# Performance work log

Measured on AMD Instinct MI355X. Metric: run time of the kernel, lower is better.

The kernel has to match this reference:

```python
import jax, jax.numpy as jnp
import numpy as np

L, D, H, R = 8, 1024, 16, 16
HD = D // H  # head dim


def setup_inputs() -> dict:
    key = jax.random.key(0)
    ks = jax.random.split(key, 7)
    s = 0.02  # init scale for stability
    return {
        "x": jax.random.normal(ks[0], (2, 1024, D), jnp.float32),
        "Wqkv": jax.random.normal(ks[1], (L, D, 3 * D), jnp.float32) * s,
        "Aqkv": jax.random.normal(ks[2], (L, D, R), jnp.float32) * s,
        "Bqkv": jax.random.normal(ks[3], (L, R, 3 * D), jnp.float32) * s,
        "Wproj": jax.random.normal(ks[4], (L, D, D), jnp.float32) * s,
        "Aproj": jax.random.normal(ks[5], (L, D, R), jnp.float32) * s,
        "Bproj": jax.random.normal(ks[6], (L, R, D), jnp.float32) * s,
    }


def _forward(x, Wqkv, Aqkv, Bqkv, Wproj, Aproj, Bproj):
    B, S, _ = x.shape
    # causal mask [S, S]
    mask = jnp.tril(jnp.ones((S, S), bool))

    def layer(h, p):
        Wq, Aq, Bq, Wp, Ap, Bp = p
        # LoRA merge exactly as the module: p + A @ B, then dense matmul
        Wq_m = Wq + Aq @ Bq            # [D, 3D]
        Wp_m = Wp + Ap @ Bp            # [D, D]
        qkv = h @ Wq_m                 # [B, S, 3D]
        q, k, v = jnp.split(qkv, 3, axis=-1)
        q = q.reshape(B, S, H, HD).transpose(0, 2, 1, 3)  # [B,H,S,hd]
        k = k.reshape(B, S, H, HD).transpose(0, 2, 1, 3)
        v = v.reshape(B, S, H, HD).transpose(0, 2, 1, 3)
        scores = jnp.einsum("bhqd,bhkd->bhqk", q, k) / np.sqrt(HD)
        scores = jnp.where(mask, scores, jnp.finfo(scores.dtype).min)
        attn = jax.nn.softmax(scores, axis=-1)
        o = jnp.einsum("bhqk,bhkd->bhqd", attn, v)        # [B,H,S,hd]
        o = o.transpose(0, 2, 1, 3).reshape(B, S, D)
        return h + o @ Wp_m, None

    out, _ = jax.lax.scan(layer, x, (Wqkv, Aqkv, Bqkv, Wproj, Aproj, Bproj))
    return out


def reference(x, Wqkv, Aqkv, Bqkv, Wproj, Aproj, Bproj):
    return _forward(x, Wqkv, Aqkv, Bqkv, Wproj, Aproj, Bproj)
```

## Files before the change

### kernel.cpp

```cpp
#include <hip/hip_runtime.h>
#include <hip/hip_bf16.h>


typedef unsigned short ushort_t;
typedef __attribute__((ext_vector_type(8))) short bf16x8;
typedef __attribute__((ext_vector_type(4))) float f32x4;

__device__ __forceinline__ unsigned short f2bf(float f) {
    union { float f; unsigned int u; } x; x.f = f;
    unsigned int r = x.u + 0x7fffu + ((x.u >> 16) & 1u);
    return (unsigned short)(r >> 16);
}

__device__ __forceinline__ f32x4 mfma16(bf16x8 a, bf16x8 b, f32x4 c) {
    return __builtin_amdgcn_mfma_f32_16x16x32_bf16(a, b, c, 0, 0, 0);
}

typedef const __attribute__((address_space(1))) unsigned int* gas_ptr;
typedef __attribute__((address_space(3))) unsigned int* las_ptr;
__device__ __forceinline__ void lds_stage16(const void* g, void* l) {
    __builtin_amdgcn_global_load_lds((gas_ptr)(unsigned long long)g,
                                     (las_ptr)(unsigned int)(unsigned long long)l,
                                     16, 0, 0);
}

#define RORMAX(x, C)                                                           \
    x = fmaxf(x, __int_as_float(__builtin_amdgcn_mov_dpp(                      \
                     __float_as_int(x), C, 0xf, 0xf, false)));
#define RORADD(x, C)                                                           \
    x += __int_as_float(__builtin_amdgcn_mov_dpp(                              \
        __float_as_int(x), C, 0xf, 0xf, false));

__global__ __launch_bounds__(256) void convert_x(
    const float4* __restrict__ in, float4* __restrict__ outF,
    ushort4* __restrict__ outB, int n4) {
    int i = blockIdx.x * 256 + threadIdx.x;
    if (i < n4) {
        float4 v = in[i];
        outF[i] = v;
        ushort4 o;
        o.x = f2bf(v.x); o.y = f2bf(v.y); o.z = f2bf(v.z); o.w = f2bf(v.w);
        outB[i] = o;
    }
}

__global__ __launch_bounds__(256) void merge_T2(
    const float* __restrict__ Wq, const float* __restrict__ Aq,
    const float* __restrict__ Bq, unsigned short* __restrict__ WTq,
    const float* __restrict__ Wp, const float* __restrict__ Ap,
    const float* __restrict__ Bp, unsigned short* __restrict__ WTp) {
    __shared__ float Asl[32][17];
    __shared__ __align__(16) float tW[32 * 128];
    int bid = blockIdx.x;
    const float *W, *A, *Bm;
    unsigned short* WT;
    int N, bx, by, bz;
    if (bid < 6144) {
        N = 3072; bx = bid % 24; int u = bid / 24; by = u & 31; bz = u >> 5;
        W = Wq; A = Aq; Bm = Bq; WT = WTq;
    } else {
        bid -= 6144;
        N = 1024; bx = bid & 7; int u = bid >> 3; by = u & 31; bz = u >> 5;
        W = Wp; A = Ap; Bm = Bp; WT = WTp;
    }
    W  += (size_t)bz * 1024 * N;
    A  += (size_t)bz * 1024 * 16;
    Bm += (size_t)bz * 16 * N;
    WT += (size_t)bz * N * 1024;
    const int j0 = bx * 128, i0 = by * 32;
    const int tid = threadIdx.x;
    const int w = tid >> 6, lane = tid & 63;

    #pragma unroll
    for (int s = 0; s < 4; s++) {
        int w4s = w * 4 + s;
        int tr = w4s * 2 + (lane >> 5);
        lds_stage16(W + (size_t)(i0 + tr) * N + j0 + (lane & 31) * 4,
                    (char*)tW + w4s * 1024);
    }
    if (tid < 128) {
        int r = tid >> 2, c4 = (tid & 3) * 4;
        float4 a = *(const float4*)&A[(size_t)(i0 + r) * 16 + c4];
        Asl[r][c4 + 0] = a.x; Asl[r][c4 + 1] = a.y;
        Asl[r][c4 + 2] = a.z; Asl[r][c4 + 3] = a.w;
    }
    const int jj = tid >> 1, half = tid & 1;
    float bcol[16];
    #pragma unroll
    for (int r = 0; r < 16; r++)
        bcol[r] = Bm[(size_t)r * N + j0 + jj];
    __builtin_amdgcn_sched_barrier(0);
    __syncthreads();

    bf16x8 o0, o1;
    #pragma unroll
    for (int c = 0; c < 16; c++) {
        int rloc = half * 16 + c;
        float v = tW[rloc * 128 + jj];
        #pragma unroll
        for (int r = 0; r < 16; r++)
            v += Asl[rloc][r] * bcol[r];
        unsigned short b = f2bf(v);
        if (c < 8) o0[c] = (short)b; else o1[c - 8] = (short)b;
    }
    unsigned short* dst = &WT[(size_t)(j0 + jj) * 1024 + i0 + half * 16];
    *(bf16x8*)dst = o0;
    *(bf16x8*)(dst + 8) = o1;
}

__global__ __launch_bounds__(256) void gemm_qkv(
    const unsigned short* __restrict__ A,
    const unsigned short* __restrict__ BT,
    unsigned short* __restrict__ outB,
    unsigned short* __restrict__ VT,
    int M, int N, int K) {
    __shared__ __align__(16) unsigned short As[2][2][64 * 32];
    __shared__ __align__(16) unsigned short Bs[2][2][128 * 32];
    const int tid = threadIdx.x;
    const int m0 = blockIdx.y * 64, n0 = blockIdx.x * 128;
    const int w = tid >> 6, lane = tid & 63;
    const int wm = (w >> 1) * 32, wn = (w & 1) * 64;
    const int lr = lane & 15, quad = lane >> 4;
    const int srowA = w * 16 + (lane >> 2);
    const int skof = (lane & 3) * 8;

    f32x4 acc[2][4] = {};

    auto stage = [&](int k0, int buf) {
        #pragma unroll
        for (int h = 0; h < 2; h++) {
            lds_stage16(A + (size_t)(m0 + srowA) * K + k0 + h * 32 + skof,
                        (char*)As[buf][h] + w * 1024);
            #pragma unroll
            for (int s = 0; s < 2; s++) {
                int srowB = w * 32 + s * 16 + (lane >> 2);
                lds_stage16(BT + (size_t)(n0 + srowB) * K + k0 + h * 32 + skof,
                            (char*)Bs[buf][h] + (w * 2 + s) * 1024);
            }
        }
    };

    const int nk = K >> 6;
    stage(0, 0);
    for (int t = 0; t < nk; t++) {
        __syncthreads();
        if (t + 1 < nk) stage((t + 1) << 6, (t + 1) & 1);
        const int cur = t & 1;
        #pragma unroll
        for (int h = 0; h < 2; h++) {
            bf16x8 af[2], bfr[4];
            #pragma unroll
            for (int i = 0; i < 2; i++)
                af[i] = *(const bf16x8*)&As[cur][h][(wm + i * 16 + lr) * 32 + quad * 8];
            #pragma unroll
            for (int j = 0; j < 4; j++)
                bfr[j] = *(const bf16x8*)&Bs[cur][h][(wn + j * 16 + lr) * 32 + quad * 8];
            #pragma unroll
            for (int i = 0; i < 2; i++)
                #pragma unroll
                for (int j = 0; j < 4; j++)
                    acc[i][j] = mfma16(af[i], bfr[j], acc[i][j]);
        }
    }
    if (n0 < 2048) {
        #pragma unroll
        for (int i = 0; i < 2; i++)
            #pragma unroll
            for (int j = 0; j < 4; j++)
                #pragma unroll
                for (int r = 0; r < 4; r++) {
                    int row = m0 + wm + i * 16 + quad * 4 + r;
                    int col = n0 + wn + j * 16 + lr;
                    float v = acc[i][j][r];
                    if (col < 1024) v *= 0.125f * 1.44269504f;
                    outB[(size_t)row * N + col] = f2bf(v);
                }
    } else {
        const int b = m0 >> 10;
        #pragma unroll
        for (int i = 0; i < 2; i++) {
            int row0 = m0 + wm + i * 16 + quad * 4;
            int s = row0 & 1023;
            #pragma unroll
            for (int j = 0; j < 4; j++) {
                int hd = n0 - 2048 + wn + j * 16 + lr;
                ushort4 o;
                o.x = f2bf(acc[i][j][0]); o.y = f2bf(acc[i][j][1]);
                o.z = f2bf(acc[i][j][2]); o.w = f2bf(acc[i][j][3]);
                *(ushort4*)&VT[((size_t)b * 1024 + hd) * 1024 + s] = o;
            }
        }
    }
}

__global__ __launch_bounds__(256) void gemm_bf16_64(
    const unsigned short* __restrict__ A,
    const unsigned short* __restrict__ BT,
    const float* __restrict__ res,
    float* __restrict__ outF,
    unsigned short* __restrict__ outB,
    int M, int N, int K) {
    __shared__ __align__(16) unsigned short As[2][2][64 * 32];
    __shared__ __align__(16) unsigned short Bs[2][2][64 * 32];
    const int tid = threadIdx.x;
    const int m0 = blockIdx.y * 64, n0 = blockIdx.x * 64;
    const int w = tid >> 6, lane = tid & 63;
    const int wm = (w >> 1) * 32, wn = (w & 1) * 32;
    const int lr = lane & 15, quad = lane >> 4;
    const int srow = w * 16 + (lane >> 2);
    const int skof = (lane & 3) * 8;

    f32x4 acc[2][2] = {};

    auto stage = [&](int k0, int buf) {
        #pragma unroll
        for (int h = 0; h < 2; h++) {
            lds_stage16(A  + (size_t)(m0 + srow) * K + k0 + h * 32 + skof,
                        (char*)As[buf][h] + w * 1024);
            lds_stage16(BT + (size_t)(n0 + srow) * K + k0 + h * 32 + skof,
                        (char*)Bs[buf][h] + w * 1024);
        }
    };

    const int nk = K >> 6;
    stage(0, 0);
    for (int t = 0; t < nk; t++) {
        __syncthreads();
        if (t + 1 < nk) stage((t + 1) << 6, (t + 1) & 1);
        const int cur = t & 1;
        #pragma unroll
        for (int h = 0; h < 2; h++) {
            bf16x8 af[2], bfr[2];
            #pragma unroll
            for (int i = 0; i < 2; i++) {
                af[i]  = *(const bf16x8*)&As[cur][h][(wm + i * 16 + lr) * 32 + quad * 8];
                bfr[i] = *(const bf16x8*)&Bs[cur][h][(wn + i * 16 + lr) * 32 + quad * 8];
            }
            #pragma unroll
            for (int i = 0; i < 2; i++)
                #pragma unroll
                for (int j = 0; j < 2; j++)
                    acc[i][j] = mfma16(af[i], bfr[j], acc[i][j]);
        }
    }
    #pragma unroll
    for (int i = 0; i < 2; i++)
        #pragma unroll
        for (int j = 0; j < 2; j++)
            #pragma unroll
            for (int r = 0; r < 4; r++) {
                int row = m0 + wm + i * 16 + quad * 4 + r;
                int col = n0 + wn + j * 16 + lr;
                float v = acc[i][j][r] + res[(size_t)row * N + col];
                if (outF) outF[(size_t)row * N + col] = v;
                if (outB) outB[(size_t)row * N + col] = f2bf(v);
            }
}

__global__ __launch_bounds__(256) void attn_kernel(
    const unsigned short* __restrict__ qkv,
    const unsigned short* __restrict__ VT,
    unsigned short* __restrict__ O) {
    __shared__ __align__(16) unsigned short Ks[2][2][64 * 32];
    __shared__ __align__(16) unsigned short Vs[2][2][64 * 32];
    __shared__ __align__(16) unsigned short pl[4][16 * 72];
    const int tid = threadIdx.x;
    const int w = tid >> 6, lane = tid & 63;
    const int lr = lane & 15, quad = lane >> 4;
    const int bh = blockIdx.y, b = bh >> 4, h = bh & 15;
    const int qblk = (bh < 16) ? blockIdx.x : (15 - blockIdx.x);
    const int qb = qblk * 64 + w * 16;
    const int srow = w * 16 + (lane >> 2);
    const int skof = (lane & 3) * 8;

    const size_t rowQ = (size_t)(b * 1024 + qb + lr) * 3072 + h * 64;
    bf16x8 aq0 = *(const bf16x8*)&qkv[rowQ + quad * 8];
    bf16x8 aq1 = *(const bf16x8*)&qkv[rowQ + 32 + quad * 8];

    float m_i[4], l_i[4];
    f32x4 oacc[4] = {};
    #pragma unroll
    for (int r = 0; r < 4; r++) { m_i[r] = -1e30f; l_i[r] = 0.f; }

    auto stage = [&](int kt64, int buf) {
        const int kt = kt64 << 6;
        const size_t gK = (size_t)(b * 1024 + kt + srow) * 3072 + 1024 + h * 64;
        lds_stage16(qkv + gK + skof,      (char*)Ks[buf][0] + w * 1024);
        lds_stage16(qkv + gK + 32 + skof, (char*)Ks[buf][1] + w * 1024);
        const size_t gV = ((size_t)bh * 64 + srow) * 1024 + kt;
        lds_stage16(VT + gV + skof,       (char*)Vs[buf][0] + w * 1024);
        lds_stage16(VT + gV + 32 + skof,  (char*)Vs[buf][1] + w * 1024);
    };

    const int nkt = qblk + 1;
    stage(0, 0);
    for (int kt64 = 0; kt64 < nkt; kt64++) {
        __syncthreads();
        if (kt64 + 1 < nkt) stage(kt64 + 1, (kt64 + 1) & 1);
        const int cur = kt64 & 1;
        const int kt = kt64 << 6;

        f32x4 s[4] = {};
        #pragma unroll
        for (int nh = 0; nh < 4; nh++) {
            bf16x8 kb0 = *(const bf16x8*)&Ks[cur][0][(nh * 16 + lr) * 32 + quad * 8];
            bf16x8 kb1 = *(const bf16x8*)&Ks[cur][1][(nh * 16 + lr) * 32 + quad * 8];
            s[nh] = mfma16(aq0, kb0, s[nh]);
            s[nh] = mfma16(aq1, kb1, s[nh]);
        }
        float mx[4];
        if (kt + 64 > qb) {
            #pragma unroll
            for (int r = 0; r < 4; r++) {
                int qrow = qb + quad * 4 + r;
                #pragma unroll
                for (int nh = 0; nh < 4; nh++) {
                    int kcol = kt + nh * 16 + lr;
                    s[nh][r] = (kcol <= qrow) ? s[nh][r] : -1e30f;
                }
            }
        }
        #pragma unroll
        for (int r = 0; r < 4; r++) {
            mx[r] = fmaxf(fmaxf(s[0][r], s[1][r]), fmaxf(s[2][r], s[3][r]));
            RORMAX(mx[r], 0x121) RORMAX(mx[r], 0x122)
            RORMAX(mx[r], 0x124) RORMAX(mx[r], 0x128)
        }
        float al[4];
        #pragma unroll
        for (int r = 0; r < 4; r++) {
            float mnew = fmaxf(m_i[r], mx[r]);
            al[r] = exp2f(m_i[r] - mnew);
            m_i[r] = mnew;
            float lsum = 0.f;
            #pragma unroll
            for (int nh = 0; nh < 4; nh++) {
                float p = exp2f(s[nh][r] - mnew);
                s[nh][r] = p;
                lsum += p;
            }
            l_i[r] = l_i[r] * al[r] + lsum;
        }
        #pragma unroll
        for (int dt = 0; dt < 4; dt++)
            #pragma unroll
            for (int r = 0; r < 4; r++) oacc[dt][r] *= al[r];
        #pragma unroll
        for (int nh = 0; nh < 4; nh++)
            #pragma unroll
            for (int r = 0; r < 4; r++)
                pl[w][(quad * 4 + r) * 72 + nh * 16 + lr] = f2bf(s[nh][r]);
        bf16x8 ap0 = *(const bf16x8*)&pl[w][lr * 72 + quad * 8];
        bf16x8 ap1 = *(const bf16x8*)&pl[w][lr * 72 + 32 + quad * 8];
        #pragma unroll
        for (int dt = 0; dt < 4; dt++) {
            bf16x8 vb0 = *(const bf16x8*)&Vs[cur][0][(dt * 16 + lr) * 32 + quad * 8];
            bf16x8 vb1 = *(const bf16x8*)&Vs[cur][1][(dt * 16 + lr) * 32 + quad * 8];
            oacc[dt] = mfma16(ap0, vb0, oacc[dt]);
            oacc[dt] = mfma16(ap1, vb1, oacc[dt]);
        }
    }
    #pragma unroll
    for (int r = 0; r < 4; r++) {
        RORADD(l_i[r], 0x121) RORADD(l_i[r], 0x122)
        RORADD(l_i[r], 0x124) RORADD(l_i[r], 0x128)
    }
    #pragma unroll
    for (int dt = 0; dt < 4; dt++)
        #pragma unroll
        for (int r = 0; r < 4; r++) {
            int row = b * 1024 + qb + quad * 4 + r;
            int col = h * 64 + dt * 16 + lr;
            O[(size_t)row * 1024 + col] = f2bf(oacc[dt][r] / l_i[r]);
        }
}

extern "C" void kernel_launch(void* const* d_in, const int* in_sizes, int n_in,
                              void* d_out, int out_size, void* d_ws, size_t ws_size,
                              hipStream_t stream) {
    const float* x     = (const float*)d_in[0];
    const float* Wqkv  = (const float*)d_in[1];
    const float* Aqkv  = (const float*)d_in[2];
    const float* Bqkv  = (const float*)d_in[3];
    const float* Wproj = (const float*)d_in[4];
    const float* Aproj = (const float*)d_in[5];
    const float* Bproj = (const float*)d_in[6];
    float* out = (float*)d_out;

    char* ws = (char*)d_ws;
    float* h_f32 = (float*)ws;                    ws += (size_t)2048 * 1024 * 4;
    unsigned short* h_bf   = (unsigned short*)ws; ws += (size_t)2048 * 1024 * 2;
    unsigned short* qkv_bf = (unsigned short*)ws; ws += (size_t)2048 * 3072 * 2;
    unsigned short* VT     = (unsigned short*)ws; ws += (size_t)32 * 64 * 1024 * 2;
    unsigned short* O_bf   = (unsigned short*)ws; ws += (size_t)2048 * 1024 * 2;
    unsigned short* WqT8   = (unsigned short*)ws; ws += (size_t)8 * 3072 * 1024 * 2;
    unsigned short* WpT8   = (unsigned short*)ws; ws += (size_t)8 * 1024 * 1024 * 2;

    convert_x<<<2048, 256, 0, stream>>>((const float4*)x, (float4*)h_f32,
                                        (ushort4*)h_bf, 2048 * 1024 / 4);
    merge_T2<<<8192, 256, 0, stream>>>(Wqkv, Aqkv, Bqkv, WqT8,
                                       Wproj, Aproj, Bproj, WpT8);

    for (int l = 0; l < 8; l++) {
        const unsigned short* WqT = WqT8 + (size_t)l * 3072 * 1024;
        const unsigned short* WpT = WpT8 + (size_t)l * 1024 * 1024;
        gemm_qkv<<<dim3(24, 32), 256, 0, stream>>>(h_bf, WqT, qkv_bf, VT,
                                                   2048, 3072, 1024);
        attn_kernel<<<dim3(16, 32), 256, 0, stream>>>(qkv_bf, VT, O_bf);
        float* outF = (l == 7) ? out : h_f32;
        gemm_bf16_64<<<dim3(16, 32), 256, 0, stream>>>(O_bf, WpT, h_f32, outF,
                                                       h_bf, 2048, 1024, 1024);
    }
}
```

Measured before the change: 682.5 us.

## Transpose QK^T MFMA in attention so softmax runs per-lane with lazy rescale

Swaps the MFMA operands for the score product so each lane holds one query row, letting the row max and sum mostly reduce within registers plus two cross-lane shuffles. Adds a threshold-based lazy rescale that skips the output rescale unless the running max grows by more than 8. Packs P to bf16 with the hardware v_cvt_pk_bf16_f32 instruction and writes it as vectors, and replaces the final division with a reciprocal multiply. Skipping the rescale lets exponentials run against a stale max, which relies on fp32 headroom; the attention kernel is only part of the total time.

Measured after the change: 664.2 us. 2.7% less time.

```diff
diff --git a/kernel.cpp b/kernel.cpp
--- a/kernel.cpp
+++ b/kernel.cpp
@@ -5,11 +5,24 @@
 typedef unsigned short ushort_t;
 typedef __attribute__((ext_vector_type(8))) short bf16x8;
 typedef __attribute__((ext_vector_type(4))) float f32x4;
+typedef __attribute__((ext_vector_type(2))) unsigned int uint32x2;
 
 __device__ __forceinline__ unsigned short f2bf(float f) {
     union { float f; unsigned int u; } x; x.f = f;
     unsigned int r = x.u + 0x7fffu + ((x.u >> 16) & 1u);
     return (unsigned short)(r >> 16);
+}
+
+__device__ __forceinline__ unsigned short f2bf_fast(float f) {
+    unsigned int r;
+    asm("v_cvt_pk_bf16_f32 %0, %1, %2" : "=v"(r) : "v"(f), "v"(0.f));
+    return (unsigned short)r;
+}
+
+__device__ __forceinline__ unsigned int cvtpk(float lo, float hi) {
+    unsigned int r;
+    asm("v_cvt_pk_bf16_f32 %0, %1, %2" : "=v"(r) : "v"(lo), "v"(hi));
+    return r;
 }
 
 __device__ __forceinline__ f32x4 mfma16(bf16x8 a, bf16x8 b, f32x4 c) {
@@ -23,13 +36,6 @@
                                      (las_ptr)(unsigned int)(unsigned long long)l,
                                      16, 0, 0);
 }
-
-#define RORMAX(x, C)                                                           \
-    x = fmaxf(x, __int_as_float(__builtin_amdgcn_mov_dpp(                      \
-                     __float_as_int(x), C, 0xf, 0xf, false)));
-#define RORADD(x, C)                                                           \
-    x += __int_as_float(__builtin_amdgcn_mov_dpp(                              \
-        __float_as_int(x), C, 0xf, 0xf, false));
 
 __global__ __launch_bounds__(256) void convert_x(
     const float4* __restrict__ in, float4* __restrict__ outF,
@@ -263,7 +269,7 @@
     unsigned short* __restrict__ O) {
     __shared__ __align__(16) unsigned short Ks[2][2][64 * 32];
     __shared__ __align__(16) unsigned short Vs[2][2][64 * 32];
-    __shared__ __align__(16) unsigned short pl[4][16 * 72];
+    __shared__ __align__(16) unsigned short pls[4][16 * 72];
     const int tid = threadIdx.x;
     const int w = tid >> 6, lane = tid & 63;
     const int lr = lane & 15, quad = lane >> 4;
@@ -277,10 +283,8 @@
     bf16x8 aq0 = *(const bf16x8*)&qkv[rowQ + quad * 8];
     bf16x8 aq1 = *(const bf16x8*)&qkv[rowQ + 32 + quad * 8];
 
-    float m_i[4], l_i[4];
+    float m_i = -1e30f, l_i = 0.f;
     f32x4 oacc[4] = {};
-    #pragma unroll
-    for (int r = 0; r < 4; r++) { m_i[r] = -1e30f; l_i[r] = 0.f; }
 
     auto stage = [&](int kt64, int buf) {
         const int kt = kt64 << 6;
@@ -305,53 +309,58 @@
         for (int nh = 0; nh < 4; nh++) {
             bf16x8 kb0 = *(const bf16x8*)&Ks[cur][0][(nh * 16 + lr) * 32 + quad * 8];
             bf16x8 kb1 = *(const bf16x8*)&Ks[cur][1][(nh * 16 + lr) * 32 + quad * 8];
-            s[nh] = mfma16(aq0, kb0, s[nh]);
-            s[nh] = mfma16(aq1, kb1, s[nh]);
-        }
-        float mx[4];
+            s[nh] = mfma16(kb0, aq0, s[nh]);
+            s[nh] = mfma16(kb1, aq1, s[nh]);
+        }
         if (kt + 64 > qb) {
-            #pragma unroll
-            for (int r = 0; r < 4; r++) {
-                int qrow = qb + quad * 4 + r;
+            const int qrow = qb + lr;
+            #pragma unroll
+            for (int nh = 0; nh < 4; nh++)
                 #pragma unroll
-                for (int nh = 0; nh < 4; nh++) {
-                    int kcol = kt + nh * 16 + lr;
+                for (int r = 0; r < 4; r++) {
+                    int kcol = kt + nh * 16 + quad * 4 + r;
                     s[nh][r] = (kcol <= qrow) ? s[nh][r] : -1e30f;
                 }
+        }
+        float mx = fmaxf(fmaxf(s[0][0], s[0][1]), fmaxf(s[0][2], s[0][3]));
+        #pragma unroll
+        for (int nh = 1; nh < 4; nh++)
+            mx = fmaxf(mx, fmaxf(fmaxf(s[nh][0], s[nh][1]),
+                                 fmaxf(s[nh][2], s[nh][3])));
+        mx = fmaxf(mx, __shfl_xor(mx, 16));
+        mx = fmaxf(mx, __shfl_xor(mx, 32));
+        if (__any(mx > m_i + 8.f)) {
+            float mnew = fmaxf(m_i, mx);
+            float al = exp2f(m_i - mnew);
+            m_i = mnew;
+            l_i *= al;
+            float alr[4];
+            #pragma unroll
+            for (int r = 0; r < 4; r++) alr[r] = __shfl(al, quad * 4 + r);
+            #pragma unroll
+            for (int dt = 0; dt < 4; dt++)
+                #pragma unroll
+                for (int r = 0; r < 4; r++) oacc[dt][r] *= alr[r];
+        }
+        float lp = 0.f;
+        #pragma unroll
+        for (int nh = 0; nh < 4; nh++)
+            #pragma unroll
+            for (int r = 0; r < 4; r++) {
+                float p = exp2f(s[nh][r] - m_i);
+                s[nh][r] = p;
+                lp += p;
             }
-        }
-        #pragma unroll
-        for (int r = 0; r < 4; r++) {
-            mx[r] = fmaxf(fmaxf(s[0][r], s[1][r]), fmaxf(s[2][r], s[3][r]));
-            RORMAX(mx[r], 0x121) RORMAX(mx[r], 0x122)
-            RORMAX(mx[r], 0x124) RORMAX(mx[r], 0x128)
-        }
-        float al[4];
-        #pragma unroll
-        for (int r = 0; r < 4; r++) {
-            float mnew = fmaxf(m_i[r], mx[r]);
-            al[r] = exp2f(m_i[r] - mnew);
-            m_i[r] = mnew;
-            float lsum = 0.f;
-            #pragma unroll
-            for (int nh = 0; nh < 4; nh++) {
-                float p = exp2f(s[nh][r] - mnew);
-                s[nh][r] = p;
-                lsum += p;
-            }
-            l_i[r] = l_i[r] * al[r] + lsum;
-        }
-        #pragma unroll
-        for (int dt = 0; dt < 4; dt++)
-            #pragma unroll
-            for (int r = 0; r < 4; r++) oacc[dt][r] *= al[r];
-        #pragma unroll
-        for (int nh = 0; nh < 4; nh++)
-            #pragma unroll
-            for (int r = 0; r < 4; r++)
-                pl[w][(quad * 4 + r) * 72 + nh * 16 + lr] = f2bf(s[nh][r]);
-        bf16x8 ap0 = *(const bf16x8*)&pl[w][lr * 72 + quad * 8];
-        bf16x8 ap1 = *(const bf16x8*)&pl[w][lr * 72 + 32 + quad * 8];
+        l_i += lp;
+        #pragma unroll
+        for (int nh = 0; nh < 4; nh++) {
+            uint32x2 pv;
+            pv[0] = cvtpk(s[nh][0], s[nh][1]);
+            pv[1] = cvtpk(s[nh][2], s[nh][3]);
+            *(uint32x2*)&pls[w][lr * 72 + nh * 16 + quad * 4] = pv;
+        }
+        bf16x8 ap0 = *(const bf16x8*)&pls[w][lr * 72 + quad * 8];
+        bf16x8 ap1 = *(const bf16x8*)&pls[w][lr * 72 + 32 + quad * 8];
         #pragma unroll
         for (int dt = 0; dt < 4; dt++) {
             bf16x8 vb0 = *(const bf16x8*)&Vs[cur][0][(dt * 16 + lr) * 32 + quad * 8];
@@ -360,18 +369,18 @@
             oacc[dt] = mfma16(ap1, vb1, oacc[dt]);
         }
     }
-    #pragma unroll
-    for (int r = 0; r < 4; r++) {
-        RORADD(l_i[r], 0x121) RORADD(l_i[r], 0x122)
-        RORADD(l_i[r], 0x124) RORADD(l_i[r], 0x128)
-    }
+    l_i += __shfl_xor(l_i, 16);
+    l_i += __shfl_xor(l_i, 32);
+    float rl[4];
+    #pragma unroll
+    for (int r = 0; r < 4; r++) rl[r] = 1.f / __shfl(l_i, quad * 4 + r);
     #pragma unroll
     for (int dt = 0; dt < 4; dt++)
         #pragma unroll
         for (int r = 0; r < 4; r++) {
             int row = b * 1024 + qb + quad * 4 + r;
             int col = h * 64 + dt * 16 + lr;
-            O[(size_t)row * 1024 + col] = f2bf(oacc[dt][r] / l_i[r]);
+            O[(size_t)row * 1024 + col] = f2bf_fast(oacc[dt][r] * rl[r]);
         }
 }
 
```
